# Performance work log

Measured on AMD Instinct MI355X. Metric: run time of the kernel, lower is better.

## Reference

```python
import jax, jax.numpy as jnp
import numpy as np

HEADS = 8
DIM_HEAD = 64
SCALE = DIM_HEAD ** -0.5


def setup_inputs() -> dict:
    key = jax.random.key(0)
    k1, k2, k3 = jax.random.split(key, 3)
    b, dim, n = 4, 256, 2048
    hidden = HEADS * DIM_HEAD  # 512
    x = jax.random.normal(k1, (b, dim, n), dtype=jnp.float32)
    # Conv1d kernel-size-1 weights are pointwise linear maps over channels.
    w_qkv = jax.random.normal(k2, (3 * hidden, dim), dtype=jnp.float32) * (dim ** -0.5)
    w_out = jax.random.normal(k3, (dim, hidden), dtype=jnp.float32) * (hidden ** -0.5)
    b_out = jnp.zeros((dim,), dtype=jnp.float32)
    return {"x": x, "w_qkv": w_qkv, "w_out": w_out, "b_out": b_out}


def reference(x, w_qkv, w_out, b_out):
    b, dim, n = x.shape
    hidden = w_out.shape[1]
    # pointwise conv1d == channel matmul: [3h, dim] x [b, dim, n] -> [b, 3h, n]
    qkv = jnp.einsum('oi,bin->bon', w_qkv, x)
    q, k, v = jnp.split(qkv, 3, axis=1)
    # b (h c) n -> b h c n
    reshape = lambda t: t.reshape(b, HEADS, DIM_HEAD, n)
    q, k, v = reshape(q) * SCALE, reshape(k), reshape(v)
    sim = jnp.einsum('bhdi,bhdj->bhij', q, k)          # [b, h, n, n]
    attn = jax.nn.softmax(sim, axis=-1)
    out = jnp.einsum('bhij,bhdj->bhid', attn, v)        # [b, h, n, d]
    # b h n d -> b (h d) n
    out = out.transpose(0, 1, 3, 2).reshape(b, hidden, n)
    return jnp.einsum('oi,bin->bon', w_out, out) + b_out[None, :, None]
```

## Files before the change

kernel.cpp:

```cpp
#include <hip/hip_runtime.h>
#include <stdint.h>

#define SEQ  2048
#define DIMC 256
#define HID  512
#define NH   8
#define DH   64

typedef __attribute__((ext_vector_type(8))) short bf16x8;
typedef __attribute__((ext_vector_type(4))) float f32x4;
typedef __attribute__((ext_vector_type(16))) float f32x16;
typedef __attribute__((ext_vector_type(2))) unsigned uint2v;
typedef __attribute__((address_space(1))) const uint32_t guint_t;
typedef __attribute__((address_space(3))) uint32_t luint_t;

__device__ __forceinline__ void gld16(const void* g, void* l) {
  __builtin_amdgcn_global_load_lds((guint_t*)g, (luint_t*)l, 16, 0, 0);
}

__device__ __forceinline__ unsigned short f2bf(float f) {
  union { float f; uint32_t u; } v; v.f = f;
  return (unsigned short)((v.u + 0x7FFFu + ((v.u >> 16) & 1u)) >> 16);
}

__device__ __forceinline__ uint32_t fbits(float f) {
  union { float f; uint32_t u; } v; v.f = f; return v.u;
}

__device__ __forceinline__ uint32_t pku(uint32_t u0, uint32_t u1) {
  return __builtin_amdgcn_perm(u1 + 0x8000u, u0 + 0x8000u, 0x07060302u);
}

__device__ __forceinline__ void swap32(uint32_t& a, uint32_t& b) {
#if __has_builtin(__builtin_amdgcn_permlane32_swap)
  uint2v r = __builtin_amdgcn_permlane32_swap(a, b, false, false);
  a = r[0]; b = r[1];
#else
  uint32_t aw = __shfl_xor(a, 32);
  uint32_t bw = __shfl_xor(b, 32);
  bool lo = (threadIdx.x & 32) == 0;
  uint32_t an = lo ? a : bw;
  uint32_t bn = lo ? aw : b;
  a = an; b = bn;
#endif
}

__global__ __launch_bounds__(256) void prep_kernel(
    const float* __restrict__ x, const float* __restrict__ wqkv,
    const float* __restrict__ wout,
    unsigned short* __restrict__ wqkv_b, unsigned short* __restrict__ wout_b,
    unsigned short* __restrict__ xT) {
  __shared__ float tile[64][65];
  int blk = blockIdx.x;
  int t = threadIdx.x;
  if (blk < 384) {
    int idx = blk * 1024 + t * 4;
    float4 v = *(const float4*)(wqkv + idx);
    float s = ((idx >> 8) < HID) ? 0.18033688011112042f : 1.0f;
    ushort4 o;
    o.x = f2bf(v.x * s); o.y = f2bf(v.y * s);
    o.z = f2bf(v.z * s); o.w = f2bf(v.w * s);
    *(ushort4*)(wqkv_b + idx) = o;
    return;
  }
  if (blk < 512) {
    int idx = (blk - 384) * 1024 + t * 4;
    float4 v = *(const float4*)(wout + idx);
    ushort4 o;
    o.x = f2bf(v.x); o.y = f2bf(v.y); o.z = f2bf(v.z); o.w = f2bf(v.w);
    *(ushort4*)(wout_b + idx) = o;
    return;
  }
  int tid = blk - 512;
  int b  = tid >> 7;
  int r  = tid & 127;
  int i0 = (r >> 5) * 64;
  int n0 = (r & 31) * 64;
  const float* xb = x + (size_t)b * DIMC * SEQ;
  int tn = t & 15, ti = t >> 4;
#pragma unroll
  for (int j = 0; j < 4; j++) {
    int il = ti + j * 16;
    float4 v = *(const float4*)(xb + (size_t)(i0 + il) * SEQ + n0 + tn * 4);
    tile[il][tn*4+0] = v.x; tile[il][tn*4+1] = v.y;
    tile[il][tn*4+2] = v.z; tile[il][tn*4+3] = v.w;
  }
  __syncthreads();
  unsigned short* xTb = xT + (size_t)b * SEQ * DIMC;
#pragma unroll
  for (int j = 0; j < 4; j++) {
    int nl = ti + j * 16;
    int i4 = tn * 4;
    uint2 pk;
    pk.x = (uint32_t)f2bf(tile[i4+0][nl]) | ((uint32_t)f2bf(tile[i4+1][nl]) << 16);
    pk.y = (uint32_t)f2bf(tile[i4+2][nl]) | ((uint32_t)f2bf(tile[i4+3][nl]) << 16);
    *(uint2*)(xTb + (size_t)(n0 + nl) * DIMC + i0 + i4) = pk;
  }
}

__global__ __launch_bounds__(256, 2) void qkv_gemm(
    const unsigned short* __restrict__ wq, const unsigned short* __restrict__ xT,
    unsigned short* __restrict__ Qs, unsigned short* __restrict__ Ks,
    unsigned short* __restrict__ Vt) {
  __shared__ unsigned short lds[17408];
  unsigned short* la = lds;
  unsigned short* lb = lds + 8192;
  int o0 = blockIdx.x * 128;
  int n0 = blockIdx.y * 128;
  int b  = blockIdx.z;
  int t  = threadIdx.x;
  int wv = t >> 6, l = t & 63, l15 = l & 15, q = l >> 4;
  int wm = (wv & 1) * 64, wn = (wv >> 1) * 64;
  f32x4 acc[4][4];
#pragma unroll
  for (int i = 0; i < 4; i++)
#pragma unroll
    for (int j = 0; j < 4; j++) acc[i][j] = (f32x4){0.f, 0.f, 0.f, 0.f};
  const unsigned short* Ag = wq + (size_t)o0 * DIMC;
  const unsigned short* Bg = xT + ((size_t)b * SEQ + n0) * DIMC;
  int lrow8 = l >> 3, lcol = l & 7;
  for (int kk = 0; kk < 4; kk++) {
    int k0 = kk * 64;
    __syncthreads();
#pragma unroll
    for (int c0 = 0; c0 < 4; c0++) {
      int c = wv * 4 + c0;
      int row = c * 8 + lrow8;
      int sg = lcol ^ (row & 7);
      gld16(Ag + (size_t)row * DIMC + k0 + sg * 8, la + c * 512);
      gld16(Bg + (size_t)row * DIMC + k0 + sg * 8, lb + c * 512);
    }
    __syncthreads();
#pragma unroll
    for (int kh = 0; kh < 2; kh++) {
      bf16x8 af[4], bfr[4];
#pragma unroll
      for (int mt = 0; mt < 4; mt++) {
        int row = wm + mt*16 + l15;
        af[mt] = *(const bf16x8*)(la + row*64 + ((kh*4 + q) ^ (row & 7)) * 8);
      }
#pragma unroll
      for (int nt = 0; nt < 4; nt++) {
        int row = wn + nt*16 + l15;
        bfr[nt] = *(const bf16x8*)(lb + row*64 + ((kh*4 + q) ^ (row & 7)) * 8);
      }
#pragma unroll
      for (int mt = 0; mt < 4; mt++)
#pragma unroll
        for (int nt = 0; nt < 4; nt++)
          acc[mt][nt] = __builtin_amdgcn_mfma_f32_16x16x32_bf16(af[mt], bfr[nt], acc[mt][nt], 0, 0, 0);
    }
  }
  __syncthreads();
  int seg3 = o0 >> 9;
  int h0   = (o0 & 511) >> 6;
  if (seg3 == 2) {
#pragma unroll
    for (int mt = 0; mt < 4; mt++)
#pragma unroll
      for (int nt = 0; nt < 4; nt++)
#pragma unroll
        for (int r = 0; r < 4; r++) {
          int ol = wm + mt * 16 + q * 4 + r;
          int h = h0 + (ol >> 6), d = ol & 63;
          int n = n0 + wn + nt * 16 + l15;
          Vt[(((size_t)b * NH + h) * DH + d) * SEQ + n] = f2bf(acc[mt][nt][r]);
        }
  } else {
    unsigned short* dst = (seg3 == 0) ? Qs : Ks;
#pragma unroll
    for (int mt = 0; mt < 4; mt++)
#pragma unroll
      for (int nt = 0; nt < 4; nt++)
#pragma unroll
        for (int r = 0; r < 4; r++) {
          int ol = wm + mt * 16 + q * 4 + r;
          int nn = wn + nt * 16 + l15;
          lds[nn * 136 + ol] = f2bf(acc[mt][nt][r]);
        }
    __syncthreads();
#pragma unroll
    for (int i = 0; i < 8; i++) {
      int idx = i * 256 + t;
      int nn  = idx >> 4;
      int olb = (idx & 15) * 8;
      uint4 v = *(const uint4*)(lds + nn * 136 + olb);
      int h = h0 + (olb >> 6), d = olb & 63;
      *(uint4*)(dst + (((size_t)b * NH + h) * SEQ + n0 + nn) * DH + d) = v;
    }
  }
}

__global__ __launch_bounds__(256, 2) void attn_kernel(
    const unsigned short* __restrict__ Qs, const unsigned short* __restrict__ Ks,
    const unsigned short* __restrict__ Vt, unsigned short* __restrict__ AO) {
  __shared__ unsigned short KV[16384];
  __shared__ float Lc[256];
  int n0 = blockIdx.x * 128;
  int bh = blockIdx.y;
  int b = bh >> 3, h = bh & 7;
  int t = threadIdx.x;
  int w = t >> 6, l = t & 63, l31 = l & 31, lh = l >> 5, l7 = l & 7;
  int cg = w >> 1, qg = w & 1;
  const unsigned short* Qg = Qs + ((size_t)bh * SEQ + n0 + qg * 64) * DH;
  bf16x8 qb[2][4];
#pragma unroll
  for (int qt = 0; qt < 2; qt++)
#pragma unroll
    for (int kc = 0; kc < 4; kc++)
      qb[qt][kc] = *(const bf16x8*)(Qg + (qt*32 + l31) * DH + kc*16 + lh*8);
  f32x16 oacc[2][2];
  float lrowp[2] = {0.f, 0.f};
#pragma unroll
  for (int qt = 0; qt < 2; qt++)
#pragma unroll
    for (int dt = 0; dt < 2; dt++)
#pragma unroll
      for (int r = 0; r < 16; r++) oacc[qt][dt][r] = 0.f;
  const unsigned short* Kst = KV + cg * 4096;
  const unsigned short* Vst = KV + 8192 + cg * 4096;
  for (int it = 0; it < 16; it++) {
    int jb = it * 64;
    __syncthreads();
    if (w < 2) {
      const unsigned short* src = Ks + ((size_t)bh * SEQ + w * 1024 + jb) * DH;
      unsigned short* dst = (unsigned short*)KV + w * 4096;
#pragma unroll
      for (int g = 0; g < 8; g++) {
        int kr = g * 8 + (l >> 3);
        gld16(src + (size_t)kr * DH + (l7 ^ (kr & 7)) * 8, dst + g * 512);
      }
    } else {
      const unsigned short* src = Vt + (size_t)bh * DH * SEQ + (w - 2) * 1024 + jb;
      unsigned short* dst = (unsigned short*)KV + 8192 + (w - 2) * 4096;
#pragma unroll
      for (int g = 0; g < 8; g++) {
        int dr = g * 8 + (l >> 3);
        gld16(src + (size_t)dr * SEQ + (l7 ^ (dr & 7)) * 8, dst + g * 512);
      }
    }
    __syncthreads();
#pragma unroll
    for (int kb = 0; kb < 64; kb += 32) {
      f32x16 st[2];
#pragma unroll
      for (int qt = 0; qt < 2; qt++)
#pragma unroll
        for (int r = 0; r < 16; r++) st[qt][r] = 0.f;
#pragma unroll
      for (int kc = 0; kc < 4; kc++) {
        bf16x8 kf = *(const bf16x8*)(Kst + (kb + l31) * 64 + (((kc*2 + lh) ^ l7)) * 8);
        st[0] = __builtin_amdgcn_mfma_f32_32x32x16_bf16(kf, qb[0][kc], st[0], 0, 0, 0);
        st[1] = __builtin_amdgcn_mfma_f32_32x32x16_bf16(kf, qb[1][kc], st[1], 0, 0, 0);
      }
      bf16x8 vf[2][2];
#pragma unroll
      for (int kc2 = 0; kc2 < 2; kc2++)
#pragma unroll
        for (int dt = 0; dt < 2; dt++)
          vf[kc2][dt] = *(const bf16x8*)(Vst + (dt*32 + l31) * 64 +
                                         ((((kb >> 3) + kc2*2 + lh) ^ l7)) * 8);
#pragma unroll
      for (int qt = 0; qt < 2; qt++) {
        float p[16];
        float s0 = 0.f;
#pragma unroll
        for (int r = 0; r < 16; r++) { p[r] = __builtin_amdgcn_exp2f(st[qt][r]); s0 += p[r]; }
        lrowp[qt] += s0;
        bf16x8 af[2];
#pragma unroll
        for (int hf = 0; hf < 2; hf++) {
          uint32_t xs[4], ys[4];
#pragma unroll
          for (int j = 0; j < 4; j++) {
            xs[j] = fbits(p[hf*8 + j]);
            ys[j] = fbits(p[hf*8 + 4 + j]);
            swap32(xs[j], ys[j]);
          }
          uint32_t d0 = pku(xs[0], xs[1]);
          uint32_t d1 = pku(xs[2], xs[3]);
          uint32_t d2 = pku(ys[0], ys[1]);
          uint32_t d3 = pku(ys[2], ys[3]);
          union { uint32_t u[4]; bf16x8 v; } cv;
          cv.u[0] = d0; cv.u[1] = d1; cv.u[2] = d2; cv.u[3] = d3;
          af[hf] = cv.v;
        }
#pragma unroll
        for (int kc2 = 0; kc2 < 2; kc2++)
#pragma unroll
          for (int dt = 0; dt < 2; dt++)
            oacc[qt][dt] = __builtin_amdgcn_mfma_f32_32x32x16_bf16(af[kc2], vf[kc2][dt], oacc[qt][dt], 0, 0, 0);
      }
    }
  }
#pragma unroll
  for (int qt = 0; qt < 2; qt++) {
    float v = lrowp[qt];
    v += __shfl_xor(v, 32);
    if (l < 32) Lc[cg * 128 + qg * 64 + qt * 32 + l31] = v;
  }
  __syncthreads();
  float* Oc = (float*)KV;
  if (cg == 1) {
#pragma unroll
    for (int qt = 0; qt < 2; qt++)
#pragma unroll
      for (int dt = 0; dt < 2; dt++)
#pragma unroll
        for (int r = 0; r < 16; r++) {
          int qrow = qg*64 + qt*32 + (r & 3) + 8*(r >> 2) + 4*lh;
          Oc[qrow * 64 + dt*32 + l31] = oacc[qt][dt][r];
        }
  }
  __syncthreads();
  if (cg == 0) {
    unsigned short* AOb = AO + (size_t)b * SEQ * HID + h * DH;
#pragma unroll
    for (int qt = 0; qt < 2; qt++)
#pragma unroll
      for (int r = 0; r < 16; r++) {
        int qrow = qg*64 + qt*32 + (r & 3) + 8*(r >> 2) + 4*lh;
        float inv = __builtin_amdgcn_rcpf(Lc[qrow] + Lc[128 + qrow]);
        int n = n0 + qrow;
#pragma unroll
        for (int dt = 0; dt < 2; dt++) {
          float val = (oacc[qt][dt][r] + Oc[qrow * 64 + dt*32 + l31]) * inv;
          AOb[(size_t)n * HID + dt*32 + l31] = f2bf(val);
        }
      }
  }
}

__global__ __launch_bounds__(256, 2) void out_gemm(
    const unsigned short* __restrict__ wo, const unsigned short* __restrict__ AO,
    const float* __restrict__ bias, float* __restrict__ out) {
  __shared__ unsigned short la[64 * 64];
  __shared__ unsigned short lb[128 * 64];
  int o0 = blockIdx.x * 64;
  int n0 = blockIdx.y * 128;
  int b  = blockIdx.z;
  int t  = threadIdx.x;
  int wv = t >> 6, l = t & 63, l15 = l & 15, q = l >> 4;
  int wm = (wv & 1) * 32, wn = (wv >> 1) * 64;
  f32x4 acc[2][4];
#pragma unroll
  for (int i = 0; i < 2; i++)
#pragma unroll
    for (int j = 0; j < 4; j++) acc[i][j] = (f32x4){0.f,0.f,0.f,0.f};
  const unsigned short* Ag = wo + (size_t)o0 * HID;
  const unsigned short* Bg = AO + ((size_t)b * SEQ + n0) * HID;
  int lrow8 = l >> 3, lcol = l & 7;
  for (int kk = 0; kk < 8; kk++) {
    int k0 = kk * 64;
    __syncthreads();
#pragma unroll
    for (int c0 = 0; c0 < 2; c0++) {
      int c = wv * 2 + c0;
      int row = c * 8 + lrow8;
      int sg = lcol ^ (row & 7);
      gld16(Ag + (size_t)row * HID + k0 + sg * 8, la + c * 512);
    }
#pragma unroll
    for (int c0 = 0; c0 < 4; c0++) {
      int c = wv * 4 + c0;
      int row = c * 8 + lrow8;
      int sg = lcol ^ (row & 7);
      gld16(Bg + (size_t)row * HID + k0 + sg * 8, lb + c * 512);
    }
    __syncthreads();
#pragma unroll
    for (int kh = 0; kh < 2; kh++) {
      bf16x8 af[2], bfr[4];
#pragma unroll
      for (int mt = 0; mt < 2; mt++) {
        int row = wm + mt*16 + l15;
        af[mt] = *(const bf16x8*)(la + row*64 + ((kh*4 + q) ^ (row & 7)) * 8);
      }
#pragma unroll
      for (int nt = 0; nt < 4; nt++) {
        int row = wn + nt*16 + l15;
        bfr[nt] = *(const bf16x8*)(lb + row*64 + ((kh*4 + q) ^ (row & 7)) * 8);
      }
#pragma unroll
      for (int mt = 0; mt < 2; mt++)
#pragma unroll
        for (int nt = 0; nt < 4; nt++)
          acc[mt][nt] = __builtin_amdgcn_mfma_f32_16x16x32_bf16(af[mt], bfr[nt], acc[mt][nt], 0,0,0);
    }
  }
#pragma unroll
  for (int mt = 0; mt < 2; mt++)
#pragma unroll
    for (int nt = 0; nt < 4; nt++)
#pragma unroll
      for (int r = 0; r < 4; r++) {
        int o2 = o0 + wm + mt*16 + q*4 + r;
        int n  = n0 + wn + nt*16 + l15;
        out[((size_t)b * DIMC + o2) * SEQ + n] = acc[mt][nt][r] + bias[o2];
      }
}

extern "C" void kernel_launch(void* const* d_in, const int* in_sizes, int n_in,
                              void* d_out, int out_size, void* d_ws, size_t ws_size,
                              hipStream_t stream) {
  const float* x    = (const float*)d_in[0];
  const float* wqkv = (const float*)d_in[1];
  const float* wout = (const float*)d_in[2];
  const float* bout = (const float*)d_in[3];
  float* out = (float*)d_out;
  char* ws = (char*)d_ws;
  unsigned short* wqkv_b = (unsigned short*)(ws);
  unsigned short* wout_b = (unsigned short*)(ws + 786432);
  unsigned short* xT     = (unsigned short*)(ws + 1048576);
  unsigned short* Qs     = (unsigned short*)(ws + 5242880);
  unsigned short* Ks     = (unsigned short*)(ws + 13631488);
  unsigned short* Vt     = (unsigned short*)(ws + 22020096);
  unsigned short* AO     = (unsigned short*)(ws + 30408704);
  prep_kernel<<<1024, 256, 0, stream>>>(x, wqkv, wout, wqkv_b, wout_b, xT);
  qkv_gemm<<<dim3(12, 16, 4), 256, 0, stream>>>(wqkv_b, xT, Qs, Ks, Vt);
  attn_kernel<<<dim3(16, 32), 256, 0, stream>>>(Qs, Ks, Vt, AO);
  out_gemm<<<dim3(4, 16, 4), 256, 0, stream>>>(wout_b, AO, bout, out);
}
```

Measured before the change: 135.2 us.

## Fuse fp32-to-bf16 prep into GEMMs and double-buffer 8-wave attention

Removes the separate prep kernel. The QKV and output GEMMs now load fp32 weights and activations directly and convert them to bf16 while staging into LDS, with the transpose of x done during staging. The attention kernel moves to 512 threads with a four-way key split and double-buffered K/V staging via async LDS loads, followed by a three-step LDS reduction of the partial outputs. The output GEMM tile shrinks to 64x64 to launch more blocks. This saves a launch and the intermediate bf16 round trip, but adds conversion ALU work and scattered 2-byte LDS stores in the GEMMs.

```diff
diff --git a/kernel.cpp b/kernel.cpp
--- a/kernel.cpp
+++ b/kernel.cpp
@@ -18,15 +18,16 @@
   __builtin_amdgcn_global_load_lds((guint_t*)g, (luint_t*)l, 16, 0, 0);
 }
 
-__device__ __forceinline__ unsigned short f2bf(float f) {
-  union { float f; uint32_t u; } v; v.f = f;
-  return (unsigned short)((v.u + 0x7FFFu + ((v.u >> 16) & 1u)) >> 16);
-}
-
 __device__ __forceinline__ uint32_t fbits(float f) {
   union { float f; uint32_t u; } v; v.f = f; return v.u;
 }
-
+__device__ __forceinline__ unsigned short f2bf(float f) {
+  uint32_t u = fbits(f);
+  return (unsigned short)((u + 0x7FFFu + ((u >> 16) & 1u)) >> 16);
+}
+__device__ __forceinline__ unsigned short f2bf_fast(float f) {
+  return (unsigned short)((fbits(f) + 0x8000u) >> 16);
+}
 __device__ __forceinline__ uint32_t pku(uint32_t u0, uint32_t u1) {
   return __builtin_amdgcn_perm(u1 + 0x8000u, u0 + 0x8000u, 0x07060302u);
 }
@@ -45,61 +46,8 @@
 #endif
 }
 
-__global__ __launch_bounds__(256) void prep_kernel(
-    const float* __restrict__ x, const float* __restrict__ wqkv,
-    const float* __restrict__ wout,
-    unsigned short* __restrict__ wqkv_b, unsigned short* __restrict__ wout_b,
-    unsigned short* __restrict__ xT) {
-  __shared__ float tile[64][65];
-  int blk = blockIdx.x;
-  int t = threadIdx.x;
-  if (blk < 384) {
-    int idx = blk * 1024 + t * 4;
-    float4 v = *(const float4*)(wqkv + idx);
-    float s = ((idx >> 8) < HID) ? 0.18033688011112042f : 1.0f;
-    ushort4 o;
-    o.x = f2bf(v.x * s); o.y = f2bf(v.y * s);
-    o.z = f2bf(v.z * s); o.w = f2bf(v.w * s);
-    *(ushort4*)(wqkv_b + idx) = o;
-    return;
-  }
-  if (blk < 512) {
-    int idx = (blk - 384) * 1024 + t * 4;
-    float4 v = *(const float4*)(wout + idx);
-    ushort4 o;
-    o.x = f2bf(v.x); o.y = f2bf(v.y); o.z = f2bf(v.z); o.w = f2bf(v.w);
-    *(ushort4*)(wout_b + idx) = o;
-    return;
-  }
-  int tid = blk - 512;
-  int b  = tid >> 7;
-  int r  = tid & 127;
-  int i0 = (r >> 5) * 64;
-  int n0 = (r & 31) * 64;
-  const float* xb = x + (size_t)b * DIMC * SEQ;
-  int tn = t & 15, ti = t >> 4;
-#pragma unroll
-  for (int j = 0; j < 4; j++) {
-    int il = ti + j * 16;
-    float4 v = *(const float4*)(xb + (size_t)(i0 + il) * SEQ + n0 + tn * 4);
-    tile[il][tn*4+0] = v.x; tile[il][tn*4+1] = v.y;
-    tile[il][tn*4+2] = v.z; tile[il][tn*4+3] = v.w;
-  }
-  __syncthreads();
-  unsigned short* xTb = xT + (size_t)b * SEQ * DIMC;
-#pragma unroll
-  for (int j = 0; j < 4; j++) {
-    int nl = ti + j * 16;
-    int i4 = tn * 4;
-    uint2 pk;
-    pk.x = (uint32_t)f2bf(tile[i4+0][nl]) | ((uint32_t)f2bf(tile[i4+1][nl]) << 16);
-    pk.y = (uint32_t)f2bf(tile[i4+2][nl]) | ((uint32_t)f2bf(tile[i4+3][nl]) << 16);
-    *(uint2*)(xTb + (size_t)(n0 + nl) * DIMC + i0 + i4) = pk;
-  }
-}
-
 __global__ __launch_bounds__(256, 2) void qkv_gemm(
-    const unsigned short* __restrict__ wq, const unsigned short* __restrict__ xT,
+    const float* __restrict__ wqkv, const float* __restrict__ x,
     unsigned short* __restrict__ Qs, unsigned short* __restrict__ Ks,
     unsigned short* __restrict__ Vt) {
   __shared__ unsigned short lds[17408];
@@ -111,24 +59,47 @@
   int t  = threadIdx.x;
   int wv = t >> 6, l = t & 63, l15 = l & 15, q = l >> 4;
   int wm = (wv & 1) * 64, wn = (wv >> 1) * 64;
+  float sc = (o0 < HID) ? 0.18033688011112042f : 1.0f;
   f32x4 acc[4][4];
 #pragma unroll
   for (int i = 0; i < 4; i++)
 #pragma unroll
     for (int j = 0; j < 4; j++) acc[i][j] = (f32x4){0.f, 0.f, 0.f, 0.f};
-  const unsigned short* Ag = wq + (size_t)o0 * DIMC;
-  const unsigned short* Bg = xT + ((size_t)b * SEQ + n0) * DIMC;
-  int lrow8 = l >> 3, lcol = l & 7;
+  const float* Ag = wqkv + (size_t)o0 * DIMC;
+  const float* Bx = x + (size_t)b * DIMC * SEQ;
+  int rowA = t >> 1, halfA = t & 1;
   for (int kk = 0; kk < 4; kk++) {
     int k0 = kk * 64;
     __syncthreads();
-#pragma unroll
-    for (int c0 = 0; c0 < 4; c0++) {
-      int c = wv * 4 + c0;
-      int row = c * 8 + lrow8;
-      int sg = lcol ^ (row & 7);
-      gld16(Ag + (size_t)row * DIMC + k0 + sg * 8, la + c * 512);
-      gld16(Bg + (size_t)row * DIMC + k0 + sg * 8, lb + c * 512);
+    {
+      const float* src = Ag + (size_t)rowA * DIMC + k0 + halfA * 32;
+      float4 f[8];
+#pragma unroll
+      for (int j = 0; j < 8; j++) f[j] = ((const float4*)src)[j];
+#pragma unroll
+      for (int jj = 0; jj < 4; jj++) {
+        uint4 o;
+        o.x = pku(fbits(f[2*jj].x * sc),   fbits(f[2*jj].y * sc));
+        o.y = pku(fbits(f[2*jj].z * sc),   fbits(f[2*jj].w * sc));
+        o.z = pku(fbits(f[2*jj+1].x * sc), fbits(f[2*jj+1].y * sc));
+        o.w = pku(fbits(f[2*jj+1].z * sc), fbits(f[2*jj+1].w * sc));
+        int s = halfA * 4 + jj;
+        *(uint4*)(la + rowA * 64 + ((s ^ (rowA & 7)) * 8)) = o;
+      }
+    }
+    {
+      int k = l;
+      const float* src = Bx + (size_t)(k0 + k) * SEQ + n0 + wv * 32;
+      int s = k >> 3, k7 = k & 7;
+#pragma unroll
+      for (int j = 0; j < 8; j++) {
+        float4 f = ((const float4*)src)[j];
+        int n = wv * 32 + j * 4;
+        lb[(n+0) * 64 + ((s ^ ((n+0) & 7)) * 8) + k7] = f2bf_fast(f.x);
+        lb[(n+1) * 64 + ((s ^ ((n+1) & 7)) * 8) + k7] = f2bf_fast(f.y);
+        lb[(n+2) * 64 + ((s ^ ((n+2) & 7)) * 8) + k7] = f2bf_fast(f.z);
+        lb[(n+3) * 64 + ((s ^ ((n+3) & 7)) * 8) + k7] = f2bf_fast(f.w);
+      }
     }
     __syncthreads();
 #pragma unroll
@@ -191,17 +162,19 @@
   }
 }
 
-__global__ __launch_bounds__(256, 2) void attn_kernel(
+__global__ __launch_bounds__(512, 2) void attn_kernel(
     const unsigned short* __restrict__ Qs, const unsigned short* __restrict__ Ks,
     const unsigned short* __restrict__ Vt, unsigned short* __restrict__ AO) {
-  __shared__ unsigned short KV[16384];
-  __shared__ float Lc[256];
+  __shared__ unsigned short KV[32768];
+  __shared__ float Lc[512];
   int n0 = blockIdx.x * 128;
   int bh = blockIdx.y;
   int b = bh >> 3, h = bh & 7;
   int t = threadIdx.x;
-  int w = t >> 6, l = t & 63, l31 = l & 31, lh = l >> 5, l7 = l & 7;
-  int cg = w >> 1, qg = w & 1;
+  int w = t >> 6, l = t & 63, l31 = l & 31, lh = l >> 5;
+  int sc_ = w & 3;
+  int qg  = w >> 2;
+  int stgK = (w < 4);
   const unsigned short* Qg = Qs + ((size_t)bh * SEQ + n0 + qg * 64) * DH;
   bf16x8 qb[2][4];
 #pragma unroll
@@ -217,181 +190,209 @@
     for (int dt = 0; dt < 2; dt++)
 #pragma unroll
       for (int r = 0; r < 16; r++) oacc[qt][dt][r] = 0.f;
-  const unsigned short* Kst = KV + cg * 4096;
-  const unsigned short* Vst = KV + 8192 + cg * 4096;
+  const unsigned short* Kgs = Ks + ((size_t)bh * SEQ + sc_ * 512) * DH;
+  const unsigned short* Vgs = Vt + (size_t)bh * DH * SEQ + sc_ * 512;
+  int hv = 0;
+  auto stage = [&](int it, int buf) {
+    unsigned short* base = KV + buf * 16384 + sc_ * 2048 + (stgK ? 0 : 8192);
+    if (stgK) {
+#pragma unroll
+      for (int g = 0; g < 4; g++) {
+        int kr = g * 8 + (l >> 3);
+        gld16(Kgs + (size_t)(it*32 + kr) * DH + ((l & 7) ^ (kr & 7)) * 8,
+              base + g * 512);
+      }
+    } else {
+#pragma unroll
+      for (int g = 0; g < 4; g++) {
+        int dr = g * 16 + (l >> 2);
+        int seg = (l & 3) ^ ((dr ^ (dr >> 2)) & 3);
+        gld16(Vgs + (size_t)dr * SEQ + it*32 + seg * 8, base + g * 512);
+      }
+    }
+  };
+  stage(0, 0);
+  __syncthreads();
   for (int it = 0; it < 16; it++) {
-    int jb = it * 64;
-    __syncthreads();
-    if (w < 2) {
-      const unsigned short* src = Ks + ((size_t)bh * SEQ + w * 1024 + jb) * DH;
-      unsigned short* dst = (unsigned short*)KV + w * 4096;
-#pragma unroll
-      for (int g = 0; g < 8; g++) {
-        int kr = g * 8 + (l >> 3);
-        gld16(src + (size_t)kr * DH + (l7 ^ (kr & 7)) * 8, dst + g * 512);
-      }
-    } else {
-      const unsigned short* src = Vt + (size_t)bh * DH * SEQ + (w - 2) * 1024 + jb;
-      unsigned short* dst = (unsigned short*)KV + 8192 + (w - 2) * 4096;
-#pragma unroll
-      for (int g = 0; g < 8; g++) {
-        int dr = g * 8 + (l >> 3);
-        gld16(src + (size_t)dr * SEQ + (l7 ^ (dr & 7)) * 8, dst + g * 512);
-      }
-    }
-    __syncthreads();
-#pragma unroll
-    for (int kb = 0; kb < 64; kb += 32) {
-      f32x16 st[2];
-#pragma unroll
-      for (int qt = 0; qt < 2; qt++)
-#pragma unroll
-        for (int r = 0; r < 16; r++) st[qt][r] = 0.f;
-#pragma unroll
-      for (int kc = 0; kc < 4; kc++) {
-        bf16x8 kf = *(const bf16x8*)(Kst + (kb + l31) * 64 + (((kc*2 + lh) ^ l7)) * 8);
-        st[0] = __builtin_amdgcn_mfma_f32_32x32x16_bf16(kf, qb[0][kc], st[0], 0, 0, 0);
-        st[1] = __builtin_amdgcn_mfma_f32_32x32x16_bf16(kf, qb[1][kc], st[1], 0, 0, 0);
-      }
-      bf16x8 vf[2][2];
+    if (it + 1 < 16) stage(it + 1, (it + 1) & 1);
+    const unsigned short* Kb = KV + (it & 1) * 16384 + sc_ * 2048;
+    const unsigned short* Vb = Kb + 8192;
+    f32x16 st[2];
+#pragma unroll
+    for (int qt = 0; qt < 2; qt++)
+#pragma unroll
+      for (int r = 0; r < 16; r++) st[qt][r] = 0.f;
+#pragma unroll
+    for (int kc = 0; kc < 4; kc++) {
+      bf16x8 kf = *(const bf16x8*)(Kb + l31 * 64 + (((kc*2 + lh) ^ (l31 & 7))) * 8);
+      st[0] = __builtin_amdgcn_mfma_f32_32x32x16_bf16(kf, qb[0][kc], st[0], 0, 0, 0);
+      st[1] = __builtin_amdgcn_mfma_f32_32x32x16_bf16(kf, qb[1][kc], st[1], 0, 0, 0);
+    }
+    bf16x8 vf[2][2];
+#pragma unroll
+    for (int kc2 = 0; kc2 < 2; kc2++)
+#pragma unroll
+      for (int dt = 0; dt < 2; dt++) {
+        int d = dt*32 + l31;
+        hv = (d ^ (d >> 2)) & 3;
+        vf[kc2][dt] = *(const bf16x8*)(Vb + d * 32 + (((kc2*2 + lh) ^ hv)) * 8);
+      }
+#pragma unroll
+    for (int qt = 0; qt < 2; qt++) {
+      float p[16];
+      float s0 = 0.f;
+#pragma unroll
+      for (int r = 0; r < 16; r++) { p[r] = __builtin_amdgcn_exp2f(st[qt][r]); s0 += p[r]; }
+      lrowp[qt] += s0;
+      bf16x8 af[2];
+#pragma unroll
+      for (int hf = 0; hf < 2; hf++) {
+        uint32_t xs[4], ys[4];
+#pragma unroll
+        for (int j = 0; j < 4; j++) {
+          xs[j] = fbits(p[hf*8 + j]);
+          ys[j] = fbits(p[hf*8 + 4 + j]);
+          swap32(xs[j], ys[j]);
+        }
+        union { uint32_t u[4]; bf16x8 v; } cv;
+        cv.u[0] = pku(xs[0], xs[1]);
+        cv.u[1] = pku(xs[2], xs[3]);
+        cv.u[2] = pku(ys[0], ys[1]);
+        cv.u[3] = pku(ys[2], ys[3]);
+        af[hf] = cv.v;
+      }
 #pragma unroll
       for (int kc2 = 0; kc2 < 2; kc2++)
 #pragma unroll
         for (int dt = 0; dt < 2; dt++)
-          vf[kc2][dt] = *(const bf16x8*)(Vst + (dt*32 + l31) * 64 +
-                                         ((((kb >> 3) + kc2*2 + lh) ^ l7)) * 8);
-#pragma unroll
-      for (int qt = 0; qt < 2; qt++) {
-        float p[16];
-        float s0 = 0.f;
-#pragma unroll
-        for (int r = 0; r < 16; r++) { p[r] = __builtin_amdgcn_exp2f(st[qt][r]); s0 += p[r]; }
-        lrowp[qt] += s0;
-        bf16x8 af[2];
-#pragma unroll
-        for (int hf = 0; hf < 2; hf++) {
-          uint32_t xs[4], ys[4];
-#pragma unroll
-          for (int j = 0; j < 4; j++) {
-            xs[j] = fbits(p[hf*8 + j]);
-            ys[j] = fbits(p[hf*8 + 4 + j]);
-            swap32(xs[j], ys[j]);
-          }
-          uint32_t d0 = pku(xs[0], xs[1]);
-          uint32_t d1 = pku(xs[2], xs[3]);
-          uint32_t d2 = pku(ys[0], ys[1]);
-          uint32_t d3 = pku(ys[2], ys[3]);
-          union { uint32_t u[4]; bf16x8 v; } cv;
-          cv.u[0] = d0; cv.u[1] = d1; cv.u[2] = d2; cv.u[3] = d3;
-          af[hf] = cv.v;
-        }
-#pragma unroll
-        for (int kc2 = 0; kc2 < 2; kc2++)
-#pragma unroll
-          for (int dt = 0; dt < 2; dt++)
-            oacc[qt][dt] = __builtin_amdgcn_mfma_f32_32x32x16_bf16(af[kc2], vf[kc2][dt], oacc[qt][dt], 0, 0, 0);
-      }
-    }
+          oacc[qt][dt] = __builtin_amdgcn_mfma_f32_32x32x16_bf16(af[kc2], vf[kc2][dt], oacc[qt][dt], 0, 0, 0);
+    }
+    __syncthreads();
   }
 #pragma unroll
   for (int qt = 0; qt < 2; qt++) {
     float v = lrowp[qt];
     v += __shfl_xor(v, 32);
-    if (l < 32) Lc[cg * 128 + qg * 64 + qt * 32 + l31] = v;
-  }
+    if (l < 32) Lc[sc_ * 128 + qg * 64 + qt * 32 + l31] = v;
+  }
+  float* Ocf = (float*)KV;
+  auto dump = [&](float* R) {
+#pragma unroll
+    for (int qt = 0; qt < 2; qt++)
+#pragma unroll
+      for (int dt = 0; dt < 2; dt++)
+#pragma unroll
+        for (int rr = 0; rr < 4; rr++)
+          *(f32x4*)(R + ((qt*2+dt)*4 + rr) * 256 + l * 4) =
+            (f32x4){oacc[qt][dt][rr*4+0], oacc[qt][dt][rr*4+1],
+                    oacc[qt][dt][rr*4+2], oacc[qt][dt][rr*4+3]};
+  };
+  auto addin = [&](const float* R) {
+#pragma unroll
+    for (int qt = 0; qt < 2; qt++)
+#pragma unroll
+      for (int dt = 0; dt < 2; dt++)
+#pragma unroll
+        for (int rr = 0; rr < 4; rr++) {
+          f32x4 v = *(const f32x4*)(R + ((qt*2+dt)*4 + rr) * 256 + l * 4);
+          oacc[qt][dt][rr*4+0] += v[0]; oacc[qt][dt][rr*4+1] += v[1];
+          oacc[qt][dt][rr*4+2] += v[2]; oacc[qt][dt][rr*4+3] += v[3];
+        }
+  };
+  if (sc_ & 1) dump(Ocf + qg * 8192 + (sc_ >> 1) * 4096);
   __syncthreads();
-  float* Oc = (float*)KV;
-  if (cg == 1) {
-#pragma unroll
-    for (int qt = 0; qt < 2; qt++)
-#pragma unroll
-      for (int dt = 0; dt < 2; dt++)
-#pragma unroll
-        for (int r = 0; r < 16; r++) {
-          int qrow = qg*64 + qt*32 + (r & 3) + 8*(r >> 2) + 4*lh;
-          Oc[qrow * 64 + dt*32 + l31] = oacc[qt][dt][r];
-        }
-  }
+  if (!(sc_ & 1)) addin(Ocf + qg * 8192 + (sc_ >> 1) * 4096);
   __syncthreads();
-  if (cg == 0) {
+  if (sc_ == 2) dump(Ocf + qg * 8192);
+  __syncthreads();
+  if (sc_ == 0) {
+    addin(Ocf + qg * 8192);
     unsigned short* AOb = AO + (size_t)b * SEQ * HID + h * DH;
 #pragma unroll
     for (int qt = 0; qt < 2; qt++)
 #pragma unroll
       for (int r = 0; r < 16; r++) {
         int qrow = qg*64 + qt*32 + (r & 3) + 8*(r >> 2) + 4*lh;
-        float inv = __builtin_amdgcn_rcpf(Lc[qrow] + Lc[128 + qrow]);
+        float lsum = Lc[qrow] + Lc[128 + qrow] + Lc[256 + qrow] + Lc[384 + qrow];
+        float inv = __builtin_amdgcn_rcpf(lsum);
         int n = n0 + qrow;
 #pragma unroll
-        for (int dt = 0; dt < 2; dt++) {
-          float val = (oacc[qt][dt][r] + Oc[qrow * 64 + dt*32 + l31]) * inv;
-          AOb[(size_t)n * HID + dt*32 + l31] = f2bf(val);
-        }
+        for (int dt = 0; dt < 2; dt++)
+          AOb[(size_t)n * HID + dt*32 + l31] = f2bf(oacc[qt][dt][r] * inv);
       }
   }
 }
 
 __global__ __launch_bounds__(256, 2) void out_gemm(
-    const unsigned short* __restrict__ wo, const unsigned short* __restrict__ AO,
+    const float* __restrict__ wo, const unsigned short* __restrict__ AO,
     const float* __restrict__ bias, float* __restrict__ out) {
   __shared__ unsigned short la[64 * 64];
-  __shared__ unsigned short lb[128 * 64];
+  __shared__ unsigned short lb[64 * 64];
   int o0 = blockIdx.x * 64;
-  int n0 = blockIdx.y * 128;
+  int n0 = blockIdx.y * 64;
   int b  = blockIdx.z;
   int t  = threadIdx.x;
   int wv = t >> 6, l = t & 63, l15 = l & 15, q = l >> 4;
-  int wm = (wv & 1) * 32, wn = (wv >> 1) * 64;
-  f32x4 acc[2][4];
+  int wm = (wv & 1) * 32, wn = (wv >> 1) * 32;
+  f32x4 acc[2][2];
 #pragma unroll
   for (int i = 0; i < 2; i++)
 #pragma unroll
-    for (int j = 0; j < 4; j++) acc[i][j] = (f32x4){0.f,0.f,0.f,0.f};
-  const unsigned short* Ag = wo + (size_t)o0 * HID;
+    for (int j = 0; j < 2; j++) acc[i][j] = (f32x4){0.f,0.f,0.f,0.f};
+  const float* Ag = wo + (size_t)o0 * HID;
   const unsigned short* Bg = AO + ((size_t)b * SEQ + n0) * HID;
-  int lrow8 = l >> 3, lcol = l & 7;
+  int rowA = t >> 2, q4 = t & 3;
   for (int kk = 0; kk < 8; kk++) {
     int k0 = kk * 64;
     __syncthreads();
+    {
+      const float* src = Ag + (size_t)rowA * HID + k0 + q4 * 16;
+      float4 f[4];
+#pragma unroll
+      for (int j = 0; j < 4; j++) f[j] = ((const float4*)src)[j];
+#pragma unroll
+      for (int jj = 0; jj < 2; jj++) {
+        uint4 o;
+        o.x = pku(fbits(f[2*jj].x),   fbits(f[2*jj].y));
+        o.y = pku(fbits(f[2*jj].z),   fbits(f[2*jj].w));
+        o.z = pku(fbits(f[2*jj+1].x), fbits(f[2*jj+1].y));
+        o.w = pku(fbits(f[2*jj+1].z), fbits(f[2*jj+1].w));
+        int s = q4 * 2 + jj;
+        *(uint4*)(la + rowA * 64 + ((s ^ (rowA & 7)) * 8)) = o;
+      }
+    }
 #pragma unroll
     for (int c0 = 0; c0 < 2; c0++) {
       int c = wv * 2 + c0;
-      int row = c * 8 + lrow8;
-      int sg = lcol ^ (row & 7);
-      gld16(Ag + (size_t)row * HID + k0 + sg * 8, la + c * 512);
-    }
-#pragma unroll
-    for (int c0 = 0; c0 < 4; c0++) {
-      int c = wv * 4 + c0;
-      int row = c * 8 + lrow8;
-      int sg = lcol ^ (row & 7);
+      int row = c * 8 + (l >> 3);
+      int sg = (l & 7) ^ (row & 7);
       gld16(Bg + (size_t)row * HID + k0 + sg * 8, lb + c * 512);
     }
     __syncthreads();
 #pragma unroll
     for (int kh = 0; kh < 2; kh++) {
-      bf16x8 af[2], bfr[4];
+      bf16x8 af[2], bfr[2];
 #pragma unroll
       for (int mt = 0; mt < 2; mt++) {
         int row = wm + mt*16 + l15;
         af[mt] = *(const bf16x8*)(la + row*64 + ((kh*4 + q) ^ (row & 7)) * 8);
       }
 #pragma unroll
-      for (int nt = 0; nt < 4; nt++) {
+      for (int nt = 0; nt < 2; nt++) {
         int row = wn + nt*16 + l15;
         bfr[nt] = *(const bf16x8*)(lb + row*64 + ((kh*4 + q) ^ (row & 7)) * 8);
       }
 #pragma unroll
       for (int mt = 0; mt < 2; mt++)
 #pragma unroll
-        for (int nt = 0; nt < 4; nt++)
+        for (int nt = 0; nt < 2; nt++)
           acc[mt][nt] = __builtin_amdgcn_mfma_f32_16x16x32_bf16(af[mt], bfr[nt], acc[mt][nt], 0,0,0);
     }
   }
 #pragma unroll
   for (int mt = 0; mt < 2; mt++)
 #pragma unroll
-    for (int nt = 0; nt < 4; nt++)
+    for (int nt = 0; nt < 2; nt++)
 #pragma unroll
       for (int r = 0; r < 4; r++) {
         int o2 = o0 + wm + mt*16 + q*4 + r;
@@ -409,15 +410,11 @@
   const float* bout = (const float*)d_in[3];
   float* out = (float*)d_out;
   char* ws = (char*)d_ws;
-  unsigned short* wqkv_b = (unsigned short*)(ws);
-  unsigned short* wout_b = (unsigned short*)(ws + 786432);
-  unsigned short* xT     = (unsigned short*)(ws + 1048576);
-  unsigned short* Qs     = (unsigned short*)(ws + 5242880);
-  unsigned short* Ks     = (unsigned short*)(ws + 13631488);
-  unsigned short* Vt     = (unsigned short*)(ws + 22020096);
-  unsigned short* AO     = (unsigned short*)(ws + 30408704);
-  prep_kernel<<<1024, 256, 0, stream>>>(x, wqkv, wout, wqkv_b, wout_b, xT);
-  qkv_gemm<<<dim3(12, 16, 4), 256, 0, stream>>>(wqkv_b, xT, Qs, Ks, Vt);
-  attn_kernel<<<dim3(16, 32), 256, 0, stream>>>(Qs, Ks, Vt, AO);
-  out_gemm<<<dim3(4, 16, 4), 256, 0, stream>>>(wout_b, AO, bout, out);
-}
+  unsigned short* Qs = (unsigned short*)(ws);
+  unsigned short* Ks = (unsigned short*)(ws + 8388608);
+  unsigned short* Vt = (unsigned short*)(ws + 16777216);
+  unsigned short* AO = (unsigned short*)(ws + 25165824);
+  qkv_gemm<<<dim3(12, 16, 4), 256, 0, stream>>>(wqkv, x, Qs, Ks, Vt);
+  attn_kernel<<<dim3(16, 32), 512, 0, stream>>>(Qs, Ks, Vt, AO);
+  out_gemm<<<dim3(4, 32, 4), 256, 0, stream>>>(wout, AO, bout, out);
+}
```

New measurement: 169.4 us. 25.3% more time.
